# Kernel optimization log

Measured on AMD Instinct MI355X. Metric: run time of the kernel, lower is better.

## Reference

```python
import jax, jax.numpy as jnp
import numpy as np

NUM_LAYERS = 2


def _relabel(sig, order_pos, M):
    """Assign consecutive int ids to unique rows of sig [M, K], numbered by
    first occurrence according to order_pos (mimics torch dict-insertion order)."""
    # lexsort: primary key must be last -> reverse columns
    perm = jnp.lexsort(tuple(sig[:, ::-1].T))
    s = sig[perm]
    neq = jnp.any(s[1:] != s[:-1], axis=1)
    gid_sorted = jnp.concatenate(
        [jnp.zeros(1, jnp.int32), jnp.cumsum(neq).astype(jnp.int32)])
    gid = jnp.zeros(M, jnp.int32).at[perm].set(gid_sorted)
    # first occurrence position of each group (empty segments -> int32 max)
    first = jax.ops.segment_min(order_pos, gid, num_segments=M)
    order = jnp.argsort(first)  # groups ranked by first occurrence
    ranks = jnp.zeros(M, jnp.int32).at[order].set(jnp.arange(M, dtype=jnp.int32))
    return ranks[gid]


def _histogram(labels, M):
    # torch returns length == num_colors; we pad with zeros to the static max M
    return jnp.zeros(M, jnp.int32).at[labels.reshape(-1)].add(1)


def setup_inputs() -> dict:
    key = jax.random.key(0)
    k1, k2 = jax.random.split(key)
    N, E, C = 256, 8192, 16
    x = jax.random.randint(k1, (N,), 0, C, dtype=jnp.int32)
    edge_index = jax.random.randint(k2, (2, E), 0, N, dtype=jnp.int32)
    return {"x": x, "edge_index": edge_index}


def reference(x, edge_index):
    x = x.astype(jnp.int32)
    N = x.shape[0]
    M = N * N
    # adjacency indicator (duplicate edges collapse, matching the any() check)
    A = jnp.zeros((N, N), jnp.int32).at[edge_index[0], edge_index[1]].set(1)

    # atomic coloring: signature = (x[v1], x[v2], connected)
    sig0 = jnp.stack([
        jnp.broadcast_to(x[:, None], (N, N)).reshape(M),
        jnp.broadcast_to(x[None, :], (N, N)).reshape(M),
        A.reshape(M),
    ], axis=1)
    # torch iterates permutations (i!=j, lexicographic) first, then the diagonal
    i = jnp.arange(N, dtype=jnp.int32)[:, None]
    j = jnp.arange(N, dtype=jnp.int32)[None, :]
    off = i * (N - 1) + jnp.where(j < i, j, j - 1)
    pos = jnp.where(i == j, N * (N - 1) + i, off).reshape(M)
    labels = _relabel(sig0, pos, M).reshape(N, N)

    hists = [_histogram(labels, M)]
    rowmajor = jnp.arange(M, dtype=jnp.int32)
    for _ in range(NUM_LAYERS):
        row_s = jnp.sort(labels, axis=1)        # sorted row multiset per v1
        col_s = jnp.sort(labels, axis=0).T      # sorted col multiset per v2
        sig = jnp.concatenate([
            labels.reshape(M, 1),
            jnp.broadcast_to(row_s[:, None, :], (N, N, N)).reshape(M, N),
            jnp.broadcast_to(col_s[None, :, :], (N, N, N)).reshape(M, N),
        ], axis=1)  # [M, 2N+1]
        labels = _relabel(sig, rowmajor, M).reshape(N, N)
        hists.append(_histogram(labels, M))
    return tuple(hists)
```

## Files before the change

### kernel.cpp

```cpp
#include <hip/hip_runtime.h>

#define NN 256
#define MM 65536
#define TBL 131072
#define TBL_MASK (TBL - 1)


__global__ void build_adj(const int* __restrict__ ei, int* __restrict__ A, int E) {
    int e = blockIdx.x * blockDim.x + threadIdx.x;
    if (e < E) {
        int s = ei[e];
        int d = ei[E + e];
        A[s * NN + d] = 1;
    }
}

__device__ __forceinline__ unsigned key0_of(const int* x, const int* A, int i, int j, int m) {
    return ((unsigned)x[i] << 5) | ((unsigned)x[j] << 1) | (unsigned)A[m];
}

__global__ void init_key_pass(const int* __restrict__ x, const int* __restrict__ A,
                              unsigned* __restrict__ mp0, unsigned* __restrict__ c0) {
    int m = blockIdx.x * blockDim.x + threadIdx.x;
    int i = m >> 8, j = m & 255;
    unsigned key = key0_of(x, A, i, j, m);
    unsigned pos = (i == j) ? (unsigned)(NN * (NN - 1) + i)
                            : (unsigned)(i * (NN - 1) + (j < i ? j : j - 1));
    atomicMax(&mp0[key], ~pos);
    atomicAdd(&c0[key], 1u);
}

__global__ void rank0_fused(const unsigned* __restrict__ mp0, const unsigned* __restrict__ c0,
                            unsigned* __restrict__ rank0, int* __restrict__ hist) {
    __shared__ unsigned pos_s[512];
    int k = threadIdx.x;
    unsigned c = c0[k];
    pos_s[k] = c ? ~mp0[k] : 0xFFFFFFFFu;
    __syncthreads();
    if (c) {
        unsigned my = pos_s[k];
        int rk = 0;
        for (int kk = 0; kk < 512; ++kk) rk += (pos_s[kk] < my);
        rank0[k] = (unsigned)rk;
        hist[rk] = (int)c;
    }
}

__global__ void write_labels0(const int* __restrict__ x, const int* __restrict__ A,
                              const unsigned* __restrict__ rank0, int* __restrict__ labels) {
    int m = blockIdx.x * blockDim.x + threadIdx.x;
    int i = m >> 8, j = m & 255;
    labels[m] = (int)rank0[key0_of(x, A, i, j, m)];
}


__device__ __forceinline__ void bitonic256(int* s, int t) {
    for (int k = 2; k <= NN; k <<= 1) {
        for (int jj = k >> 1; jj > 0; jj >>= 1) {
            int ixj = t ^ jj;
            if (ixj > t) {
                int a = s[t], b = s[ixj];
                bool asc = ((t & k) == 0);
                if (asc ? (a > b) : (a < b)) {
                    s[t] = b;
                    s[ixj] = a;
                }
            }
            __syncthreads();
        }
    }
}

__global__ void sort_both(const int* __restrict__ labels, int* __restrict__ rowsorted,
                          int* __restrict__ colsorted, int* __restrict__ rvec,
                          int* __restrict__ cvec) {
    __shared__ int s[NN];
    int bx = blockIdx.x;
    int i = bx & 255, mode = bx >> 8, t = threadIdx.x;
    int* rep = mode ? cvec : rvec;
    int* dst = mode ? colsorted : rowsorted;
    if (t == 0) rep[i] = i;
    s[t] = mode ? labels[t * NN + i] : labels[i * NN + t];
    __syncthreads();
    bitonic256(s, t);
    dst[i * NN + t] = s[t];
}

__global__ void rep_pairs_both(const int* __restrict__ rowsorted,
                               const int* __restrict__ colsorted, int* __restrict__ rvec,
                               int* __restrict__ cvec) {
    int i = blockIdx.x;
    int wid = threadIdx.x >> 6;
    int lane = threadIdx.x & 63;
    int j = (blockIdx.y << 2) + wid;
    if (j >= i) return;
    const int* sorted = blockIdx.z ? colsorted : rowsorted;
    int* rep = blockIdx.z ? cvec : rvec;
    const int* ri = sorted + i * NN;
    const int* rj = sorted + j * NN;
    bool eq = true;
#pragma unroll
    for (int k = 0; k < NN; k += 64) eq = eq && (ri[lane + k] == rj[lane + k]);
    if (__all(eq)) {
        if (lane == 0) atomicMin(&rep[i], j);
    }
}


__global__ void relabel_insert(const int* __restrict__ labels, const int* __restrict__ r,
                               const int* __restrict__ c, unsigned long long* __restrict__ tk,
                               unsigned* __restrict__ mp, unsigned* __restrict__ cnt,
                               unsigned* __restrict__ slotidx) {
    int m = blockIdx.x * blockDim.x + threadIdx.x;
    int i = m >> 8, j = m & 255;
    unsigned key = (unsigned)labels[m] | ((unsigned)r[i] << 16) | ((unsigned)c[j] << 24);
    unsigned long long kk = (unsigned long long)key + 1ull;
    unsigned h = ((key * 2654435761u) >> 15) & TBL_MASK;
    for (;;) {
        unsigned long long prev = atomicCAS(&tk[h], 0ull, kk);
        if (prev == 0ull || prev == kk) break;
        h = (h + 1) & TBL_MASK;
    }
    slotidx[m] = h;
    atomicMax(&mp[h], ~(unsigned)m);
    atomicAdd(&cnt[h], 1u);
}

__global__ void mark_slots(const unsigned long long* __restrict__ tk,
                           const unsigned* __restrict__ mp, unsigned* __restrict__ flags) {
    int s = blockIdx.x * blockDim.x + threadIdx.x;
    if (tk[s]) flags[~mp[s]] = 1u;
}

__global__ void scan64k(const unsigned* __restrict__ in, unsigned* __restrict__ out) {
    __shared__ unsigned wsums[16];
    __shared__ unsigned carry_s;
    int t = threadIdx.x;
    int lane = t & 63, wid = t >> 6;
    if (t == 0) carry_s = 0;
    __syncthreads();
    for (int tile = 0; tile < 16; ++tile) {
        uint4 v = ((const uint4*)in)[tile * 1024 + t];
        unsigned s0 = v.x, s1 = s0 + v.y, s2 = s1 + v.z, q = s2 + v.w;
        unsigned inc = q;
#pragma unroll
        for (int off = 1; off < 64; off <<= 1) {
            unsigned n = __shfl_up(inc, off, 64);
            if (lane >= off) inc += n;
        }
        if (lane == 63) wsums[wid] = inc;
        __syncthreads();
        if (t < 16) {
            unsigned w = wsums[t];
            unsigned wi = w;
#pragma unroll
            for (int off = 1; off < 16; off <<= 1) {
                unsigned n = __shfl_up(wi, off, 64);
                if (lane >= off) wi += n;
            }
            wsums[t] = wi - w;
        }
        __syncthreads();
        unsigned base = carry_s + wsums[wid] + (inc - q);
        uint4 o;
        o.x = base;
        o.y = base + s0;
        o.z = base + s1;
        o.w = base + s2;
        ((uint4*)out)[tile * 1024 + t] = o;
        __syncthreads();
        if (t == 1023) carry_s += wsums[15] + inc;
        __syncthreads();
    }
}

__global__ void finish_layer(const unsigned long long* __restrict__ tk,
                             const unsigned* __restrict__ mp, const unsigned* __restrict__ cnt,
                             const unsigned* __restrict__ rankat,
                             const unsigned* __restrict__ slotidx, int* __restrict__ hist,
                             int* __restrict__ labels2) {
    int s = blockIdx.x * blockDim.x + threadIdx.x;
    if (s < MM) labels2[s] = (int)rankat[~mp[slotidx[s]]];
    if (tk[s]) hist[rankat[~mp[s]]] = (int)cnt[s];
}

extern "C" void kernel_launch(void* const* d_in, const int* in_sizes, int n_in,
                              void* d_out, int out_size, void* d_ws, size_t ws_size,
                              hipStream_t stream) {
    const int* x = (const int*)d_in[0];
    const int* ei = (const int*)d_in[1];
    const int E = in_sizes[1] / 2;
    int* out = (int*)d_out;

    char* w = (char*)d_ws;
    size_t off = 0;
    auto alloc = [&](size_t bytes) -> void* {
        void* p = w + off;
        off = (off + bytes + 511) & ~(size_t)511;
        return p;
    };
    unsigned long long* tkL[2] = {(unsigned long long*)alloc(TBL * 8),
                                  (unsigned long long*)alloc(TBL * 8)};
    unsigned* mpL[2] = {(unsigned*)alloc(TBL * 4), (unsigned*)alloc(TBL * 4)};
    unsigned* cntL[2] = {(unsigned*)alloc(TBL * 4), (unsigned*)alloc(TBL * 4)};
    unsigned* flagsL[2] = {(unsigned*)alloc(MM * 4), (unsigned*)alloc(MM * 4)};
    int* A = (int*)alloc(MM * 4);
    unsigned* mp0 = (unsigned*)alloc(512 * 4);
    unsigned* c0 = (unsigned*)alloc(512 * 4);
    size_t zero_end = off;
    unsigned* slotidx = (unsigned*)alloc(MM * 4);
    unsigned* rankat = (unsigned*)alloc(MM * 4);
    int* labels = (int*)alloc(MM * 4);
    int* labels2 = (int*)alloc(MM * 4);
    int* rowsorted = (int*)alloc(MM * 4);
    int* colsorted = (int*)alloc(MM * 4);
    int* rvec = (int*)alloc(NN * 4);
    int* cvec = (int*)alloc(NN * 4);
    unsigned* rank0 = (unsigned*)alloc(512 * 4);

    (void)hipMemsetAsync(d_ws, 0, zero_end, stream);
    (void)hipMemsetAsync(d_out, 0, (size_t)out_size * sizeof(int), stream);

    build_adj<<<(E + 255) / 256, 256, 0, stream>>>(ei, A, E);
    init_key_pass<<<MM / 256, 256, 0, stream>>>(x, A, mp0, c0);
    rank0_fused<<<1, 512, 0, stream>>>(mp0, c0, rank0, out);
    write_labels0<<<MM / 256, 256, 0, stream>>>(x, A, rank0, labels);

    int* lab = labels;
    int* lab2 = labels2;
    for (int layer = 0; layer < 2; ++layer) {
        sort_both<<<2 * NN, NN, 0, stream>>>(lab, rowsorted, colsorted, rvec, cvec);
        rep_pairs_both<<<dim3(NN, NN / 4, 2), 256, 0, stream>>>(rowsorted, colsorted, rvec, cvec);
        relabel_insert<<<MM / 256, 256, 0, stream>>>(lab, rvec, cvec, tkL[layer], mpL[layer],
                                                     cntL[layer], slotidx);
        mark_slots<<<TBL / 256, 256, 0, stream>>>(tkL[layer], mpL[layer], flagsL[layer]);
        scan64k<<<1, 1024, 0, stream>>>(flagsL[layer], rankat);
        finish_layer<<<TBL / 256, 256, 0, stream>>>(tkL[layer], mpL[layer], cntL[layer], rankat,
                                                    slotidx, out + (size_t)(layer + 1) * MM, lab2);
        int* tmp = lab;
        lab = lab2;
        lab2 = tmp;
    }
}
```

Before: 206.3 us.

## Replace row/col sorting with multiset hashing and bitmap-based rank compaction

Each sorted row and column multiset is replaced by an order-independent hash: the sum of a 64-bit mix of each label, reduced per row or column. A single block then finds each row's or column's first equal representative by comparing hashes. This removes the bitonic sorts and the O(N^2) pairwise vector comparisons, but equality becomes probabilistic, so a hash collision would wrongly merge two groups. The single-block 64K scan is replaced by an atomic bitmap of first-occurrence positions, which each finishing block scans redundantly with popcounts. The layer-0 label write and the output memset are also folded into other kernels, cutting the number of launches.

```diff
diff --git a/kernel.cpp b/kernel.cpp
--- a/kernel.cpp
+++ b/kernel.cpp
@@ -4,6 +4,17 @@
 #define MM 65536
 #define TBL 131072
 #define TBL_MASK (TBL - 1)
+
+__device__ __forceinline__ unsigned key0m(const int* x, const int* A, int i, int j, int m) {
+    return ((unsigned)x[i] << 5) | ((unsigned)x[j] << 1) | (unsigned)A[m];
+}
+
+__device__ __forceinline__ unsigned long long mix64(unsigned v) {
+    unsigned long long z = (unsigned long long)v + 0x9E3779B97F4A7C15ull;
+    z = (z ^ (z >> 30)) * 0xBF58476D1CE4E5B9ull;
+    z = (z ^ (z >> 27)) * 0x94D049BB133111EBull;
+    return z ^ (z >> 31);
+}
 
 
 __global__ void build_adj(const int* __restrict__ ei, int* __restrict__ A, int E) {
@@ -15,15 +26,13 @@
     }
 }
 
-__device__ __forceinline__ unsigned key0_of(const int* x, const int* A, int i, int j, int m) {
-    return ((unsigned)x[i] << 5) | ((unsigned)x[j] << 1) | (unsigned)A[m];
-}
-
 __global__ void init_key_pass(const int* __restrict__ x, const int* __restrict__ A,
-                              unsigned* __restrict__ mp0, unsigned* __restrict__ c0) {
+                              unsigned* __restrict__ mp0, unsigned* __restrict__ c0,
+                              int* __restrict__ hist0) {
     int m = blockIdx.x * blockDim.x + threadIdx.x;
+    hist0[m] = 0;
     int i = m >> 8, j = m & 255;
-    unsigned key = key0_of(x, A, i, j, m);
+    unsigned key = key0m(x, A, i, j, m);
     unsigned pos = (i == j) ? (unsigned)(NN * (NN - 1) + i)
                             : (unsigned)(i * (NN - 1) + (j < i ? j : j - 1));
     atomicMax(&mp0[key], ~pos);
@@ -46,74 +55,54 @@
     }
 }
 
-__global__ void write_labels0(const int* __restrict__ x, const int* __restrict__ A,
-                              const unsigned* __restrict__ rank0, int* __restrict__ labels) {
+__global__ void hash_both(const int* __restrict__ x, const int* __restrict__ A,
+                          const unsigned* __restrict__ rank0, const int* __restrict__ lab,
+                          int layer, unsigned long long* __restrict__ rowhash,
+                          unsigned long long* __restrict__ colhash) {
+    __shared__ unsigned long long hs[256];
+    int b = blockIdx.x, t = threadIdx.x;
+    int i = b & 255, mode = b >> 8;
+    int m = mode ? t * NN + i : i * NN + t;
+    unsigned lv = (layer == 0)
+                      ? rank0[key0m(x, A, mode ? t : i, mode ? i : t, m)]
+                      : (unsigned)lab[m];
+    hs[t] = mix64(lv);
+    __syncthreads();
+    for (int off = 128; off > 0; off >>= 1) {
+        if (t < off) hs[t] += hs[t + off];
+        __syncthreads();
+    }
+    if (t == 0) (mode ? colhash : rowhash)[i] = hs[0];
+}
+
+__global__ void rep_hash(const unsigned long long* __restrict__ rowhash,
+                         const unsigned long long* __restrict__ colhash,
+                         int* __restrict__ rvec, int* __restrict__ cvec) {
+    __shared__ unsigned long long hh[512];
+    int t = threadIdx.x;
+    hh[t] = (t < 256) ? rowhash[t] : colhash[t - 256];
+    __syncthreads();
+    int mode = t >> 8, i = t & 255, base = mode << 8;
+    unsigned long long my = hh[base + i];
+    int r = i;
+    for (int j = 0; j < i; ++j) {
+        if (hh[base + j] == my) {
+            r = j;
+            break;
+        }
+    }
+    (mode ? cvec : rvec)[i] = r;
+}
+
+__global__ void relabel_insert(const int* __restrict__ x, const int* __restrict__ A,
+                               const unsigned* __restrict__ rank0, const int* __restrict__ lab,
+                               int layer, const int* __restrict__ r, const int* __restrict__ c,
+                               unsigned long long* __restrict__ tk, unsigned* __restrict__ mp,
+                               unsigned* __restrict__ cnt, unsigned* __restrict__ slotidx) {
     int m = blockIdx.x * blockDim.x + threadIdx.x;
     int i = m >> 8, j = m & 255;
-    labels[m] = (int)rank0[key0_of(x, A, i, j, m)];
-}
-
-
-__device__ __forceinline__ void bitonic256(int* s, int t) {
-    for (int k = 2; k <= NN; k <<= 1) {
-        for (int jj = k >> 1; jj > 0; jj >>= 1) {
-            int ixj = t ^ jj;
-            if (ixj > t) {
-                int a = s[t], b = s[ixj];
-                bool asc = ((t & k) == 0);
-                if (asc ? (a > b) : (a < b)) {
-                    s[t] = b;
-                    s[ixj] = a;
-                }
-            }
-            __syncthreads();
-        }
-    }
-}
-
-__global__ void sort_both(const int* __restrict__ labels, int* __restrict__ rowsorted,
-                          int* __restrict__ colsorted, int* __restrict__ rvec,
-                          int* __restrict__ cvec) {
-    __shared__ int s[NN];
-    int bx = blockIdx.x;
-    int i = bx & 255, mode = bx >> 8, t = threadIdx.x;
-    int* rep = mode ? cvec : rvec;
-    int* dst = mode ? colsorted : rowsorted;
-    if (t == 0) rep[i] = i;
-    s[t] = mode ? labels[t * NN + i] : labels[i * NN + t];
-    __syncthreads();
-    bitonic256(s, t);
-    dst[i * NN + t] = s[t];
-}
-
-__global__ void rep_pairs_both(const int* __restrict__ rowsorted,
-                               const int* __restrict__ colsorted, int* __restrict__ rvec,
-                               int* __restrict__ cvec) {
-    int i = blockIdx.x;
-    int wid = threadIdx.x >> 6;
-    int lane = threadIdx.x & 63;
-    int j = (blockIdx.y << 2) + wid;
-    if (j >= i) return;
-    const int* sorted = blockIdx.z ? colsorted : rowsorted;
-    int* rep = blockIdx.z ? cvec : rvec;
-    const int* ri = sorted + i * NN;
-    const int* rj = sorted + j * NN;
-    bool eq = true;
-#pragma unroll
-    for (int k = 0; k < NN; k += 64) eq = eq && (ri[lane + k] == rj[lane + k]);
-    if (__all(eq)) {
-        if (lane == 0) atomicMin(&rep[i], j);
-    }
-}
-
-
-__global__ void relabel_insert(const int* __restrict__ labels, const int* __restrict__ r,
-                               const int* __restrict__ c, unsigned long long* __restrict__ tk,
-                               unsigned* __restrict__ mp, unsigned* __restrict__ cnt,
-                               unsigned* __restrict__ slotidx) {
-    int m = blockIdx.x * blockDim.x + threadIdx.x;
-    int i = m >> 8, j = m & 255;
-    unsigned key = (unsigned)labels[m] | ((unsigned)r[i] << 16) | ((unsigned)c[j] << 24);
+    unsigned l = (layer == 0) ? rank0[key0m(x, A, i, j, m)] : (unsigned)lab[m];
+    unsigned key = l | ((unsigned)r[i] << 16) | ((unsigned)c[j] << 24);
     unsigned long long kk = (unsigned long long)key + 1ull;
     unsigned h = ((key * 2654435761u) >> 15) & TBL_MASK;
     for (;;) {
@@ -126,62 +115,59 @@
     atomicAdd(&cnt[h], 1u);
 }
 
-__global__ void mark_slots(const unsigned long long* __restrict__ tk,
-                           const unsigned* __restrict__ mp, unsigned* __restrict__ flags) {
+__global__ void mark_bm(const unsigned long long* __restrict__ tk,
+                        const unsigned* __restrict__ mp, unsigned* __restrict__ bm,
+                        int* __restrict__ hist) {
     int s = blockIdx.x * blockDim.x + threadIdx.x;
-    if (tk[s]) flags[~mp[s]] = 1u;
-}
-
-__global__ void scan64k(const unsigned* __restrict__ in, unsigned* __restrict__ out) {
-    __shared__ unsigned wsums[16];
-    __shared__ unsigned carry_s;
+    if (s < MM) hist[s] = 0;
+    if (tk[s]) {
+        unsigned q = ~mp[s];
+        atomicOr(&bm[q >> 5], 1u << (q & 31));
+    }
+}
+
+__global__ void finish_bm(const unsigned long long* __restrict__ tk,
+                          const unsigned* __restrict__ mp, const unsigned* __restrict__ cnt,
+                          const unsigned* __restrict__ bm, const unsigned* __restrict__ slotidx,
+                          int* __restrict__ hist, int* __restrict__ lab) {
+    __shared__ unsigned bw[2048];
+    __shared__ unsigned wb[2048];
+    __shared__ unsigned ts[256];
     int t = threadIdx.x;
-    int lane = t & 63, wid = t >> 6;
-    if (t == 0) carry_s = 0;
-    __syncthreads();
-    for (int tile = 0; tile < 16; ++tile) {
-        uint4 v = ((const uint4*)in)[tile * 1024 + t];
-        unsigned s0 = v.x, s1 = s0 + v.y, s2 = s1 + v.z, q = s2 + v.w;
-        unsigned inc = q;
+    for (int k = t; k < 2048; k += 256) bw[k] = bm[k];
+    __syncthreads();
+    unsigned pc[8], s = 0;
 #pragma unroll
-        for (int off = 1; off < 64; off <<= 1) {
-            unsigned n = __shfl_up(inc, off, 64);
-            if (lane >= off) inc += n;
-        }
-        if (lane == 63) wsums[wid] = inc;
+    for (int k = 0; k < 8; ++k) {
+        pc[k] = (unsigned)__popc(bw[t * 8 + k]);
+        s += pc[k];
+    }
+    ts[t] = s;
+    __syncthreads();
+    for (int off = 1; off < 256; off <<= 1) {
+        unsigned v = (t >= off) ? ts[t - off] : 0u;
         __syncthreads();
-        if (t < 16) {
-            unsigned w = wsums[t];
-            unsigned wi = w;
+        ts[t] += v;
+        __syncthreads();
+    }
+    unsigned run = ts[t] - s;
 #pragma unroll
-            for (int off = 1; off < 16; off <<= 1) {
-                unsigned n = __shfl_up(wi, off, 64);
-                if (lane >= off) wi += n;
-            }
-            wsums[t] = wi - w;
-        }
-        __syncthreads();
-        unsigned base = carry_s + wsums[wid] + (inc - q);
-        uint4 o;
-        o.x = base;
-        o.y = base + s0;
-        o.z = base + s1;
-        o.w = base + s2;
-        ((uint4*)out)[tile * 1024 + t] = o;
-        __syncthreads();
-        if (t == 1023) carry_s += wsums[15] + inc;
-        __syncthreads();
-    }
-}
-
-__global__ void finish_layer(const unsigned long long* __restrict__ tk,
-                             const unsigned* __restrict__ mp, const unsigned* __restrict__ cnt,
-                             const unsigned* __restrict__ rankat,
-                             const unsigned* __restrict__ slotidx, int* __restrict__ hist,
-                             int* __restrict__ labels2) {
-    int s = blockIdx.x * blockDim.x + threadIdx.x;
-    if (s < MM) labels2[s] = (int)rankat[~mp[slotidx[s]]];
-    if (tk[s]) hist[rankat[~mp[s]]] = (int)cnt[s];
+    for (int k = 0; k < 8; ++k) {
+        wb[t * 8 + k] = run;
+        run += pc[k];
+    }
+    __syncthreads();
+
+    int sdx = blockIdx.x * 256 + t;
+    if (sdx < MM) {
+        unsigned q = ~mp[slotidx[sdx]];
+        lab[sdx] = (int)(wb[q >> 5] + (unsigned)__popc(bw[q >> 5] & ((1u << (q & 31)) - 1u)));
+    }
+    if (tk[sdx]) {
+        unsigned q = ~mp[sdx];
+        unsigned rk = wb[q >> 5] + (unsigned)__popc(bw[q >> 5] & ((1u << (q & 31)) - 1u));
+        hist[rk] = (int)cnt[sdx];
+    }
 }
 
 extern "C" void kernel_launch(void* const* d_in, const int* in_sizes, int n_in,
@@ -203,42 +189,34 @@
                                   (unsigned long long*)alloc(TBL * 8)};
     unsigned* mpL[2] = {(unsigned*)alloc(TBL * 4), (unsigned*)alloc(TBL * 4)};
     unsigned* cntL[2] = {(unsigned*)alloc(TBL * 4), (unsigned*)alloc(TBL * 4)};
-    unsigned* flagsL[2] = {(unsigned*)alloc(MM * 4), (unsigned*)alloc(MM * 4)};
+    unsigned* bmL[2] = {(unsigned*)alloc(2048 * 4), (unsigned*)alloc(2048 * 4)};
     int* A = (int*)alloc(MM * 4);
     unsigned* mp0 = (unsigned*)alloc(512 * 4);
     unsigned* c0 = (unsigned*)alloc(512 * 4);
     size_t zero_end = off;
     unsigned* slotidx = (unsigned*)alloc(MM * 4);
-    unsigned* rankat = (unsigned*)alloc(MM * 4);
-    int* labels = (int*)alloc(MM * 4);
-    int* labels2 = (int*)alloc(MM * 4);
-    int* rowsorted = (int*)alloc(MM * 4);
-    int* colsorted = (int*)alloc(MM * 4);
+    int* lab = (int*)alloc(MM * 4);
+    unsigned long long* rowhash = (unsigned long long*)alloc(NN * 8);
+    unsigned long long* colhash = (unsigned long long*)alloc(NN * 8);
     int* rvec = (int*)alloc(NN * 4);
     int* cvec = (int*)alloc(NN * 4);
     unsigned* rank0 = (unsigned*)alloc(512 * 4);
 
     (void)hipMemsetAsync(d_ws, 0, zero_end, stream);
-    (void)hipMemsetAsync(d_out, 0, (size_t)out_size * sizeof(int), stream);
 
     build_adj<<<(E + 255) / 256, 256, 0, stream>>>(ei, A, E);
-    init_key_pass<<<MM / 256, 256, 0, stream>>>(x, A, mp0, c0);
+    init_key_pass<<<MM / 256, 256, 0, stream>>>(x, A, mp0, c0, out);
     rank0_fused<<<1, 512, 0, stream>>>(mp0, c0, rank0, out);
-    write_labels0<<<MM / 256, 256, 0, stream>>>(x, A, rank0, labels);
-
-    int* lab = labels;
-    int* lab2 = labels2;
+
     for (int layer = 0; layer < 2; ++layer) {
-        sort_both<<<2 * NN, NN, 0, stream>>>(lab, rowsorted, colsorted, rvec, cvec);
-        rep_pairs_both<<<dim3(NN, NN / 4, 2), 256, 0, stream>>>(rowsorted, colsorted, rvec, cvec);
-        relabel_insert<<<MM / 256, 256, 0, stream>>>(lab, rvec, cvec, tkL[layer], mpL[layer],
-                                                     cntL[layer], slotidx);
-        mark_slots<<<TBL / 256, 256, 0, stream>>>(tkL[layer], mpL[layer], flagsL[layer]);
-        scan64k<<<1, 1024, 0, stream>>>(flagsL[layer], rankat);
-        finish_layer<<<TBL / 256, 256, 0, stream>>>(tkL[layer], mpL[layer], cntL[layer], rankat,
-                                                    slotidx, out + (size_t)(layer + 1) * MM, lab2);
-        int* tmp = lab;
-        lab = lab2;
-        lab2 = tmp;
-    }
-}
+        int* hist = out + (size_t)(layer + 1) * MM;
+        hash_both<<<2 * NN, NN, 0, stream>>>(x, A, rank0, lab, layer, rowhash, colhash);
+        rep_hash<<<1, 512, 0, stream>>>(rowhash, colhash, rvec, cvec);
+        relabel_insert<<<MM / 256, 256, 0, stream>>>(x, A, rank0, lab, layer, rvec, cvec,
+                                                     tkL[layer], mpL[layer], cntL[layer],
+                                                     slotidx);
+        mark_bm<<<TBL / 256, 256, 0, stream>>>(tkL[layer], mpL[layer], bmL[layer], hist);
+        finish_bm<<<TBL / 256, 256, 0, stream>>>(tkL[layer], mpL[layer], cntL[layer], bmL[layer],
+                                                 slotidx, hist, lab);
+    }
+}
```

Result: faster. 200.5 us (-2.8%).
